# Kernel tuning notes

Hardware: AMD Instinct MI355X
Metric: run time of the kernel (lower is better)

The kernel has to match this reference:

```python
import jax, jax.numpy as jnp
import numpy as np

N, D, NH, NC, B, NL = 400, 256, 4, 2, 64, 2
HD = D // NH


def _ln(x, g, b, eps=1e-5):
    mu = x.mean(-1, keepdims=True)
    var = ((x - mu) ** 2).mean(-1, keepdims=True)
    return (x - mu) * jax.lax.rsqrt(var + eps) * g + b


def _mha(q, kv, wqkv, bqkv, wo, bo):
    # torch nn.MultiheadAttention (batch_first), eval mode
    wq, wk, wv = jnp.split(wqkv, 3, axis=0)
    bq, bk, bv = jnp.split(bqkv, 3, axis=0)
    Bsz, Sq, _ = q.shape
    Sk = kv.shape[1]
    qh = (q @ wq.T + bq).reshape(Bsz, Sq, NH, HD).transpose(0, 2, 1, 3)
    kh = (kv @ wk.T + bk).reshape(Bsz, Sk, NH, HD).transpose(0, 2, 1, 3)
    vh = (kv @ wv.T + bv).reshape(Bsz, Sk, NH, HD).transpose(0, 2, 1, 3)
    scores = jnp.einsum('bhqd,bhkd->bhqk', qh, kh) / jnp.sqrt(jnp.float32(HD))
    attn = jax.nn.softmax(scores, axis=-1)
    o = jnp.einsum('bhqk,bhkd->bhqd', attn, vh)
    o = o.transpose(0, 2, 1, 3).reshape(Bsz, Sq, D)
    return o @ wo.T + bo


def setup_inputs() -> dict:
    key = jax.random.key(0)
    ks = iter(jax.random.split(key, 64))
    w = lambda *s: (jax.random.normal(next(ks), s, dtype=jnp.float32) * 0.02)
    inp = {
        'fc_matrix': jax.random.uniform(next(ks), (B, N, N), dtype=jnp.float32),
        'sc_matrix': jax.random.uniform(next(ks), (B, N, N), dtype=jnp.float32),
        'proj_w': w(D, N), 'proj_b': jnp.zeros((D,), jnp.float32),
        'enc_qkv_w': w(NL, 3 * D, D), 'enc_qkv_b': jnp.zeros((NL, 3 * D), jnp.float32),
        'enc_out_w': w(NL, D, D), 'enc_out_b': jnp.zeros((NL, D), jnp.float32),
        'enc_lin1_w': w(NL, 4 * D, D), 'enc_lin1_b': jnp.zeros((NL, 4 * D), jnp.float32),
        'enc_lin2_w': w(NL, D, 4 * D), 'enc_lin2_b': jnp.zeros((NL, D), jnp.float32),
        'enc_n1_g': jnp.ones((NL, D), jnp.float32), 'enc_n1_b': jnp.zeros((NL, D), jnp.float32),
        'enc_n2_g': jnp.ones((NL, D), jnp.float32), 'enc_n2_b': jnp.zeros((NL, D), jnp.float32),
        'gcn_w1': w(D, N), 'gcn_b1': jnp.zeros((D,), jnp.float32),
        'gcn_w2': w(D, D), 'gcn_b2': jnp.zeros((D,), jnp.float32),
        'ca1_qkv_w': w(3 * D, D), 'ca1_qkv_b': jnp.zeros((3 * D,), jnp.float32),
        'ca1_out_w': w(D, D), 'ca1_out_b': jnp.zeros((D,), jnp.float32),
        'ca1_n_g': jnp.ones((D,), jnp.float32), 'ca1_n_b': jnp.zeros((D,), jnp.float32),
        'ca2_qkv_w': w(3 * D, D), 'ca2_qkv_b': jnp.zeros((3 * D,), jnp.float32),
        'ca2_out_w': w(D, D), 'ca2_out_b': jnp.zeros((D,), jnp.float32),
        'ca2_n_g': jnp.ones((D,), jnp.float32), 'ca2_n_b': jnp.zeros((D,), jnp.float32),
        'cls_w1': w(128, N * D), 'cls_b1': jnp.zeros((128,), jnp.float32),
        'cls_w2': w(NC, 128), 'cls_b2': jnp.zeros((NC,), jnp.float32),
    }
    return inp


def reference(fc_matrix, sc_matrix, proj_w, proj_b,
              enc_qkv_w, enc_qkv_b, enc_out_w, enc_out_b,
              enc_lin1_w, enc_lin1_b, enc_lin2_w, enc_lin2_b,
              enc_n1_g, enc_n1_b, enc_n2_g, enc_n2_b,
              gcn_w1, gcn_b1, gcn_w2, gcn_b2,
              ca1_qkv_w, ca1_qkv_b, ca1_out_w, ca1_out_b, ca1_n_g, ca1_n_b,
              ca2_qkv_w, ca2_qkv_b, ca2_out_w, ca2_out_b, ca2_n_g, ca2_n_b,
              cls_w1, cls_b1, cls_w2, cls_b2):
    # ---- FC branch: input proj + 2 post-norm transformer encoder layers ----
    h = fc_matrix @ proj_w.T + proj_b  # [B,N,D]
    for l in range(NL):
        a = _mha(h, h, enc_qkv_w[l], enc_qkv_b[l], enc_out_w[l], enc_out_b[l])
        h = _ln(h + a, enc_n1_g[l], enc_n1_b[l])
        ff = jax.nn.relu(h @ enc_lin1_w[l].T + enc_lin1_b[l]) @ enc_lin2_w[l].T + enc_lin2_b[l]
        h = _ln(h + ff, enc_n2_g[l], enc_n2_b[l])
    Z_F = h

    # ---- SC branch: dense-equivalent of per-sample nonzero()+GCNConv ----
    # all entries of sc are nonzero -> edge set == dense adjacency (self-loops present,
    # so add_remaining_self_loops is a no-op). deg = in-degree (column sums of weights).
    deg = sc_matrix.sum(axis=-2)  # [B,N]
    dinv = jnp.where(deg > 0, jax.lax.rsqrt(deg), 0.0)
    An = dinv[:, :, None] * sc_matrix * dinv[:, None, :]  # An[b,i,j] = dinv_i * w_ij * dinv_j
    h1 = jnp.einsum('bij,bid->bjd', An, sc_matrix @ gcn_w1.T) + gcn_b1  # aggregate src->dst
    h1 = jax.nn.relu(h1)
    Z_S = jnp.einsum('bij,bid->bjd', An, h1 @ gcn_w2.T) + gcn_b2  # [B,N,D]

    # ---- Cross attention (eval: dropout = identity) ----
    Z_F_cross = _ln(Z_F + _mha(Z_F, Z_S, ca1_qkv_w, ca1_qkv_b, ca1_out_w, ca1_out_b), ca1_n_g, ca1_n_b)
    Z_S_cross = _ln(Z_S + _mha(Z_S, Z_F, ca2_qkv_w, ca2_qkv_b, ca2_out_w, ca2_out_b), ca2_n_g, ca2_n_b)

    Z_joint = (Z_F_cross + Z_S_cross) * 0.5
    flat = Z_joint.reshape(Z_joint.shape[0], -1)  # [B, N*D]
    logits = jax.nn.relu(flat @ cls_w1.T + cls_b1) @ cls_w2.T + cls_b2
    return logits
```

## Files before the change

kernel.cpp:

```cpp
#include <hip/hip_runtime.h>
#include <math.h>

#define NB   64
#define NN   400
#define DD   256
#define NHH  4
#define HDD  64
#define MR   25600

typedef __attribute__((ext_vector_type(8))) short bf16x8;
typedef __attribute__((ext_vector_type(4))) float f32x4;

__device__ __forceinline__ short f2bf(float x) {
    union { float f; unsigned u; } v; v.f = x;
    return (short)((v.u + 0x7FFFu + ((v.u >> 16) & 1u)) >> 16);
}
__device__ __forceinline__ float bf2f(short s) {
    union { unsigned u; float f; } v; v.u = ((unsigned)(unsigned short)s) << 16;
    return v.f;
}
__device__ __forceinline__ void gl_lds16(const void* g, void* l) {
    __builtin_amdgcn_global_load_lds(
        (const __attribute__((address_space(1))) unsigned*)g,
        (__attribute__((address_space(3))) unsigned*)l, 16, 0, 0);
}


__global__ __launch_bounds__(256) void gemm_p8(
    const short* __restrict__ A, int arows, long long sA,
    const short* __restrict__ B, int brows, long long sB,
    const float* __restrict__ bias,
    short* __restrict__ C, int crows, int crz, long long sCe,
    int M, int N, int Npad, int K, int relu)
{
    __shared__ short lds[17408];
    const int tid = threadIdx.x;
    const int z = blockIdx.z;
    const int m0 = blockIdx.x * 128, n0 = blockIdx.y * 128;
    const short* Ab = A + (size_t)z * sA;
    const short* Bb = B + (size_t)z * sB;

    const int w = tid >> 6, lane = tid & 63;
    const int quad = lane >> 4, l15 = lane & 15;
    const int wm = w & 1, wn = w >> 1;

    f32x4 acc[4][4] = {};

    const int KT = K >> 5;

    auto STAGE = [&](int buf, int kt) {
        const int gp0 = kt << 2;
        short* Al = lds + buf * 8192;
        short* Bl = Al + 4096;
#pragma unroll
        for (int i = 0; i < 4; ++i) {
            int c = i * 4 + w;
            int p = (c >> 1) & 3, hh = c & 1;
            if (c < 8)
                gl_lds16(Ab + ((size_t)(gp0 + p) * arows + m0 + hh * 64 + lane) * 8,
                         &Al[(p * 128 + hh * 64) * 8]);
            else
                gl_lds16(Bb + ((size_t)(gp0 + p) * brows + n0 + hh * 64 + lane) * 8,
                         &Bl[(p * 128 + hh * 64) * 8]);
        }
    };

    STAGE(0, 0);
    __syncthreads();
    for (int kt = 0; kt < KT; ++kt) {
        if (kt + 1 < KT) STAGE((kt + 1) & 1, kt + 1);
        const short* Al = lds + (kt & 1) * 8192;
        const short* Bl = Al + 4096;
        bf16x8 af[4], bfr[4];
#pragma unroll
        for (int mi = 0; mi < 4; ++mi)
            af[mi] = *reinterpret_cast<const bf16x8*>(
                &Al[(quad * 128 + wm * 64 + mi * 16 + l15) * 8]);
#pragma unroll
        for (int ni = 0; ni < 4; ++ni)
            bfr[ni] = *reinterpret_cast<const bf16x8*>(
                &Bl[(quad * 128 + wn * 64 + ni * 16 + l15) * 8]);
#pragma unroll
        for (int mi = 0; mi < 4; ++mi)
#pragma unroll
            for (int ni = 0; ni < 4; ++ni)
                acc[mi][ni] = __builtin_amdgcn_mfma_f32_16x16x32_bf16(af[mi], bfr[ni], acc[mi][ni], 0, 0, 0);
        __syncthreads();
    }

#pragma unroll
    for (int mi = 0; mi < 4; ++mi) {
#pragma unroll
        for (int r = 0; r < 4; ++r) {
            int row = wm * 64 + mi * 16 + quad * 4 + r;
#pragma unroll
            for (int ni = 0; ni < 4; ++ni) {
                int col = wn * 64 + ni * 16 + l15;
                int gcol = n0 + col;
                float v = 0.0f;
                if (gcol < N) {
                    v = acc[mi][ni][r];
                    if (bias) v += bias[gcol];
                    if (relu) v = fmaxf(v, 0.0f);
                }
                lds[row * 136 + col] = f2bf(v);
            }
        }
    }
    __syncthreads();
    short* Cbz = C + (size_t)z * sCe;
    const long long zr = (long long)z * crz;
#pragma unroll
    for (int t = 0; t < 8; ++t) {
        int c = t * 256 + tid;
        int row = c & 127, p16 = c >> 7;
        int grow = m0 + row;
        int gcol0 = n0 + p16 * 8;
        if (grow < M && gcol0 < Npad) {
            bf16x8 v = *reinterpret_cast<const bf16x8*>(&lds[row * 136 + p16 * 8]);
            *reinterpret_cast<bf16x8*>(
                &Cbz[((size_t)(gcol0 >> 3) * crows + zr + grow) * 8]) = v;
        }
    }
}

__global__ __launch_bounds__(256) void gemm_ln(
    const short* __restrict__ A,
    const short* __restrict__ B, int brows,
    const float* __restrict__ bias,
    const short* __restrict__ resid,
    const float* __restrict__ g, const float* __restrict__ bb,
    short* __restrict__ out, int K)
{
    __shared__ short lds[20480];
    __shared__ float gs[256], bs[256], bi_s[256];
    __shared__ float red[2][4][64];
    const int tid = threadIdx.x;
    const int m0 = blockIdx.x * 64;
    const int w = tid >> 6, lane = tid & 63;
    const int quad = lane >> 4, l15 = lane & 15;
    gs[tid] = g[tid]; bs[tid] = bb[tid]; bi_s[tid] = bias[tid];

    f32x4 acc[16] = {};
    const int KT = K >> 5;

    auto STAGE = [&](int buf, int kt) {
        const int gp0 = kt << 2;
        short* Al = lds + buf * 10240;
        short* Bl = Al + 2048;
#pragma unroll
        for (int i = 0; i < 5; ++i) {
            int c = i * 4 + w;
            if (c < 4) {
                gl_lds16(A + ((size_t)(gp0 + c) * MR + m0 + lane) * 8, &Al[(c * 64) * 8]);
            } else {
                int cb = c - 4, p = cb >> 2, cq = cb & 3;
                gl_lds16(B + ((size_t)(gp0 + p) * brows + cq * 64 + lane) * 8,
                         &Bl[(p * 256 + cq * 64) * 8]);
            }
        }
    };

    STAGE(0, 0);
    __syncthreads();
    for (int kt = 0; kt < KT; ++kt) {
        if (kt + 1 < KT) STAGE((kt + 1) & 1, kt + 1);
        const short* Al = lds + (kt & 1) * 10240;
        const short* Bl = Al + 2048;
        bf16x8 af = *reinterpret_cast<const bf16x8*>(
            &Al[(quad * 64 + w * 16 + l15) * 8]);
#pragma unroll
        for (int ni = 0; ni < 16; ++ni) {
            bf16x8 bfr = *reinterpret_cast<const bf16x8*>(
                &Bl[(quad * 256 + ni * 16 + l15) * 8]);
            acc[ni] = __builtin_amdgcn_mfma_f32_16x16x32_bf16(af, bfr, acc[ni], 0, 0, 0);
        }
        __syncthreads();
    }

    short* rowt = lds;
#pragma unroll
    for (int ni = 0; ni < 16; ++ni) {
        int col = ni * 16 + l15;
        int part = col >> 6, idx = col & 63;
#pragma unroll
        for (int r = 0; r < 4; ++r) {
            int row = w * 16 + quad * 4 + r;
            rowt[row * 264 + part * 66 + idx] = f2bf(acc[ni][r] + bi_s[col]);
        }
    }
    __syncthreads();

    const int row = tid >> 2, part = tid & 3;
    const int grow = m0 + row;
    float vv[8][8];
    float sum = 0.0f, sq = 0.0f;
#pragma unroll
    for (int i = 0; i < 8; ++i) {
        int plane = part * 8 + i;
        bf16x8 rv = *reinterpret_cast<const bf16x8*>(resid + ((size_t)plane * MR + grow) * 8);
        bf16x8 tv = *reinterpret_cast<const bf16x8*>(&rowt[row * 264 + part * 66 + i * 8]);
#pragma unroll
        for (int e = 0; e < 8; ++e) {
            float v = bf2f(tv[e]) + bf2f(rv[e]);
            vv[i][e] = v; sum += v; sq += v * v;
        }
    }
    red[0][part][row] = sum; red[1][part][row] = sq;
    __syncthreads();
    sum = red[0][0][row] + red[0][1][row] + red[0][2][row] + red[0][3][row];
    sq  = red[1][0][row] + red[1][1][row] + red[1][2][row] + red[1][3][row];
    float mu = sum * (1.0f / 256.0f);
    float var = sq * (1.0f / 256.0f) - mu * mu;
    float rstd = 1.0f / sqrtf(fmaxf(var, 0.0f) + 1e-5f);
#pragma unroll
    for (int i = 0; i < 8; ++i) {
        int plane = part * 8 + i;
        bf16x8 o;
#pragma unroll
        for (int e = 0; e < 8; ++e)
            o[e] = f2bf((vv[i][e] - mu) * rstd * gs[plane * 8 + e] + bs[plane * 8 + e]);
        *reinterpret_cast<bf16x8*>(out + ((size_t)plane * MR + grow) * 8) = o;
    }
}

__global__ __launch_bounds__(256) void vtrans(
    const short* __restrict__ qkv, short* __restrict__ vT)
{
    __shared__ short tile[64][66];
    const int c = blockIdx.x, h = blockIdx.y, b = blockIdx.z;
    const int tid = threadIdx.x;
    const size_t bh = (size_t)b * NHH + h;
    for (int t = tid; t < 512; t += 256) {
        int pp = t >> 6, l = t & 63;
        int j = c * 64 + l;
        bf16x8 v;
        if (j < NN)
            v = *reinterpret_cast<const bf16x8*>(
                qkv + (((size_t)(64 + 8 * h + pp)) * MR + (size_t)b * NN + j) * 8);
        else { for (int e = 0; e < 8; ++e) v[e] = 0; }
#pragma unroll
        for (int e = 0; e < 8; ++e) tile[l][pp * 8 + e] = v[e];
    }
    __syncthreads();
    for (int t = tid; t < 512; t += 256) {
        int kq = t >> 6, d = t & 63;
        int kp = c * 8 + kq;
        bf16x8 o;
#pragma unroll
        for (int e = 0; e < 8; ++e) o[e] = tile[kq * 8 + e][d];
        *reinterpret_cast<bf16x8*>(vT + ((bh * 56 + kp) * 64 + d) * 8) = o;
    }
}

__global__ __launch_bounds__(256) void attn_p8(
    const short* __restrict__ qkv, const short* __restrict__ vT,
    short* __restrict__ Out)
{
    __shared__ short KP[8 * 448 * 8];
    __shared__ short QV[2][4096];
    const int qt = blockIdx.x, h = blockIdx.y, b = blockIdx.z;
    const int tid = threadIdx.x;
    const int w = tid >> 6, lane = tid & 63;
    const int quad = lane >> 4, l15 = lane & 15;
    const size_t rowb = (size_t)b * NN;
    const size_t bh = (size_t)b * NHH + h;

    for (int j = w; j < 8; j += 4)
        gl_lds16(qkv + (((size_t)(8 * h + j)) * MR + rowb + qt * 64 + lane) * 8, &QV[0][(j * 64) * 8]);
    for (int t = w; t < 56; t += 4) {
        int j = t / 7, c = t - j * 7;
        gl_lds16(qkv + (((size_t)(32 + 8 * h + j)) * MR + rowb + c * 64 + lane) * 8,
                 &KP[(j * 448 + c * 64) * 8]);
    }
    __syncthreads();

    bf16x8 aq0 = *reinterpret_cast<const bf16x8*>(&QV[0][(quad * 64 + w * 16 + l15) * 8]);
    bf16x8 aq1 = *reinterpret_cast<const bf16x8*>(&QV[0][((4 + quad) * 64 + w * 16 + l15) * 8]);
    __syncthreads();
    gl_lds16(vT + ((bh * 56 + w) * 64 + lane) * 8,       &QV[0][(w * 64) * 8]);
    gl_lds16(vT + ((bh * 56 + 4 + w) * 64 + lane) * 8,   &QV[0][((4 + w) * 64) * 8]);

    f32x4 sacc[25];
#pragma unroll
    for (int nt = 0; nt < 25; ++nt) { sacc[nt][0] = 0; sacc[nt][1] = 0; sacc[nt][2] = 0; sacc[nt][3] = 0; }
#pragma unroll
    for (int nt = 0; nt < 25; ++nt) {
        bf16x8 b0 = *reinterpret_cast<const bf16x8*>(&KP[(quad * 448 + nt * 16 + l15) * 8]);
        bf16x8 b1 = *reinterpret_cast<const bf16x8*>(&KP[((4 + quad) * 448 + nt * 16 + l15) * 8]);
        sacc[nt] = __builtin_amdgcn_mfma_f32_16x16x32_bf16(aq0, b0, sacc[nt], 0, 0, 0);
        sacc[nt] = __builtin_amdgcn_mfma_f32_16x16x32_bf16(aq1, b1, sacc[nt], 0, 0, 0);
    }

    float mx[4] = {-3e38f, -3e38f, -3e38f, -3e38f}, sm[4] = {0, 0, 0, 0};
#pragma unroll
    for (int nt = 0; nt < 25; ++nt)
#pragma unroll
        for (int r = 0; r < 4; ++r) mx[r] = fmaxf(mx[r], sacc[nt][r]);
#pragma unroll
    for (int r = 0; r < 4; ++r) {
        mx[r] = fmaxf(mx[r], __shfl_xor(mx[r], 1));
        mx[r] = fmaxf(mx[r], __shfl_xor(mx[r], 2));
        mx[r] = fmaxf(mx[r], __shfl_xor(mx[r], 4));
        mx[r] = fmaxf(mx[r], __shfl_xor(mx[r], 8));
    }
#pragma unroll
    for (int nt = 0; nt < 25; ++nt)
#pragma unroll
        for (int r = 0; r < 4; ++r) {
            float e = __expf((sacc[nt][r] - mx[r]) * 0.125f);
            sacc[nt][r] = e;
            sm[r] += e;
        }
#pragma unroll
    for (int r = 0; r < 4; ++r) {
        sm[r] += __shfl_xor(sm[r], 1);
        sm[r] += __shfl_xor(sm[r], 2);
        sm[r] += __shfl_xor(sm[r], 4);
        sm[r] += __shfl_xor(sm[r], 8);
    }
    __syncthreads();

#pragma unroll
    for (int nt = 0; nt < 25; ++nt)
#pragma unroll
        for (int r = 0; r < 4; ++r) {
            int colk = nt * 16 + l15;
            KP[((colk >> 3) * 64 + w * 16 + quad * 4 + r) * 8 + (colk & 7)] = f2bf(sacc[nt][r]);
        }
    for (int idx = tid; idx < 1024; idx += 256) KP[25600 + idx] = 0;

    f32x4 oacc[4];
#pragma unroll
    for (int dt = 0; dt < 4; ++dt) { oacc[dt][0] = 0; oacc[dt][1] = 0; oacc[dt][2] = 0; oacc[dt][3] = 0; }
    __syncthreads();

    for (int c2 = 0; c2 < 7; ++c2) {
        if (c2 < 6) {
            const int cp = (c2 + 1) * 8;
            short* dstv = QV[(c2 + 1) & 1];
            gl_lds16(vT + ((bh * 56 + cp + w) * 64 + lane) * 8,     &dstv[(w * 64) * 8]);
            gl_lds16(vT + ((bh * 56 + cp + 4 + w) * 64 + lane) * 8, &dstv[((4 + w) * 64) * 8]);
        }
        const short* Vb = QV[c2 & 1];
#pragma unroll
        for (int half = 0; half < 2; ++half) {
            const int kt = c2 * 2 + half;
            if (kt <= 12) {
                bf16x8 pa = *reinterpret_cast<const bf16x8*>(
                    &KP[((kt * 4 + quad) * 64 + w * 16 + l15) * 8]);
#pragma unroll
                for (int dt = 0; dt < 4; ++dt) {
                    bf16x8 vb = *reinterpret_cast<const bf16x8*>(
                        &Vb[((half * 4 + quad) * 64 + dt * 16 + l15) * 8]);
                    oacc[dt] = __builtin_amdgcn_mfma_f32_16x16x32_bf16(pa, vb, oacc[dt], 0, 0, 0);
                }
            }
        }
        if (c2 < 6) __syncthreads();
    }
#pragma unroll
    for (int r = 0; r < 4; ++r) {
        int row = qt * 64 + w * 16 + quad * 4 + r;
        if (row >= NN) continue;
        float inv = 1.0f / sm[r];
#pragma unroll
        for (int dt = 0; dt < 4; ++dt) {
            int col = dt * 16 + l15;
            Out[(((size_t)(8 * h + (col >> 3))) * MR + rowb + row) * 8 + (col & 7)] =
                f2bf(oacc[dt][r] * inv);
        }
    }
}

__global__ void conv_p8(const float* __restrict__ src, short* __restrict__ dst,
                        int R, int K, int Kp, int PR)
{
    const int G = Kp >> 3;
    int idx = blockIdx.x * 256 + threadIdx.x;
    if (idx >= R * G) return;
    int r = idx / G, g = idx - r * G;
    int k0 = g << 3;
    bf16x8 o;
    if (k0 + 8 <= K) {
        const float4 v0 = *reinterpret_cast<const float4*>(src + (size_t)r * K + k0);
        const float4 v1 = *reinterpret_cast<const float4*>(src + (size_t)r * K + k0 + 4);
        o[0] = f2bf(v0.x); o[1] = f2bf(v0.y); o[2] = f2bf(v0.z); o[3] = f2bf(v0.w);
        o[4] = f2bf(v1.x); o[5] = f2bf(v1.y); o[6] = f2bf(v1.z); o[7] = f2bf(v1.w);
    } else {
#pragma unroll
        for (int e = 0; e < 8; ++e) {
            int k = k0 + e;
            o[e] = (k < K) ? f2bf(src[(size_t)r * K + k]) : (short)0;
        }
    }
    *reinterpret_cast<bf16x8*>(dst + ((size_t)g * PR + r) * 8) = o;
}

__global__ __launch_bounds__(256) void w1_p8(
    const float* __restrict__ W1, short* __restrict__ Wp)
{
    __shared__ float tile[128][129];
    const int k0 = blockIdx.x * 128;
    const int tid = threadIdx.x;
    for (int t = 0; t < 16; ++t) {
        int idx = t * 256 + tid;
        int r = idx >> 5, k4 = idx & 31;
        float4 v = *(const float4*)(W1 + (size_t)r * 102400 + k0 + k4 * 4);
        tile[r][k4 * 4 + 0] = v.x; tile[r][k4 * 4 + 1] = v.y;
        tile[r][k4 * 4 + 2] = v.z; tile[r][k4 * 4 + 3] = v.w;
    }
    __syncthreads();
    for (int t = 0; t < 8; ++t) {
        int idx = t * 256 + tid;
        int pidx = idx >> 7, r = idx & 127;
        bf16x8 o;
#pragma unroll
        for (int e = 0; e < 8; ++e) o[e] = f2bf(tile[r][pidx * 8 + e]);
        *reinterpret_cast<bf16x8*>(Wp + (((size_t)(k0 >> 3) + pidx) * 128 + r) * 8) = o;
    }
}

__global__ void colsum_dinv(const float* __restrict__ sc, float* __restrict__ dinv)
{
    int b = blockIdx.y;
    int j = blockIdx.x * 256 + threadIdx.x;
    if (j >= NN) return;
    const float* p = sc + (size_t)b * NN * NN + j;
    float s = 0.0f;
    for (int i = 0; i < NN; ++i) s += p[(size_t)i * NN];
    dinv[b * NN + j] = (s > 0.0f) ? 1.0f / sqrtf(s) : 0.0f;
}

__global__ __launch_bounds__(256) void sc_prep(
    const float* __restrict__ sc, const float* __restrict__ dinv,
    short* __restrict__ scb, short* __restrict__ anT)
{
    __shared__ float tile[64][65];
    const int b = blockIdx.z;
    const int i0 = blockIdx.y * 64, j0 = blockIdx.x * 64;
    const int tid = threadIdx.x;
    const float* sb = sc + (size_t)b * NN * NN;
    short* scbb = scb + (size_t)b * 56 * 512 * 8;
    short* anTb = anT + (size_t)b * 56 * 512 * 8;
    for (int e = tid; e < 4096; e += 256) {
        int r = e >> 6, c = e & 63;
        int i = i0 + r, j = j0 + c;
        tile[r][c] = (i < NN && j < NN) ? sb[(size_t)i * NN + j] : 0.0f;
    }
    __syncthreads();
    for (int e = tid; e < 4096; e += 256) {
        int r = e >> 6, c = e & 63;
        int i = i0 + r, j = j0 + c;
        scbb[((size_t)(j >> 3) * 512 + i) * 8 + (j & 7)] = f2bf(tile[r][c]);
        float v = 0.0f;
        if (i < NN && j < NN) v = tile[r][c] * dinv[b * NN + i] * dinv[b * NN + j];
        anTb[((size_t)(i >> 3) * 512 + j) * 8 + (i & 7)] = f2bf(v);
    }
}

__global__ __launch_bounds__(256) void cls_gemm(
    const short* __restrict__ C1, const short* __restrict__ C2,
    const short* __restrict__ Wp, float* __restrict__ partial)
{
    __shared__ short Al[32 * 64 * 8];
    __shared__ short Wl[8 * 128 * 8];
    const int j = blockIdx.x;
    const int tid = threadIdx.x;
    const int w = tid >> 6, lane = tid & 63;
    const int quad = lane >> 4, l15 = lane & 15;

    for (int s = 0; s < 8; ++s) {
        int idx = s * 256 + tid;
        int p = idx >> 6, b = idx & 63;
        size_t ad = ((size_t)p * MR + (size_t)b * NN + j) * 8;
        bf16x8 a = *reinterpret_cast<const bf16x8*>(C1 + ad);
        bf16x8 c = *reinterpret_cast<const bf16x8*>(C2 + ad);
        bf16x8 o;
#pragma unroll
        for (int e = 0; e < 8; ++e) o[e] = f2bf(0.5f * (bf2f(a[e]) + bf2f(c[e])));
        *reinterpret_cast<bf16x8*>(&Al[(p * 64 + b) * 8]) = o;
    }

    f32x4 acc[4][2] = {};
    const size_t wp0 = (size_t)j * 32;
    for (int s = 0; s < 4; ++s) {
#pragma unroll
        for (int pp = 0; pp < 2; ++pp) {
            int p = w + pp * 4;
            gl_lds16(Wp + ((wp0 + s * 8 + p) * 128 + lane) * 8,      &Wl[(p * 128) * 8]);
            gl_lds16(Wp + ((wp0 + s * 8 + p) * 128 + 64 + lane) * 8, &Wl[(p * 128 + 64) * 8]);
        }
        __syncthreads();
#pragma unroll
        for (int kb = 0; kb < 2; ++kb) {
            bf16x8 af[4], bfr[2];
#pragma unroll
            for (int mi = 0; mi < 4; ++mi)
                af[mi] = *reinterpret_cast<const bf16x8*>(
                    &Al[((s * 8 + kb * 4 + quad) * 64 + mi * 16 + l15) * 8]);
#pragma unroll
            for (int ni = 0; ni < 2; ++ni)
                bfr[ni] = *reinterpret_cast<const bf16x8*>(
                    &Wl[((kb * 4 + quad) * 128 + w * 32 + ni * 16 + l15) * 8]);
#pragma unroll
            for (int mi = 0; mi < 4; ++mi)
#pragma unroll
                for (int ni = 0; ni < 2; ++ni)
                    acc[mi][ni] = __builtin_amdgcn_mfma_f32_16x16x32_bf16(af[mi], bfr[ni], acc[mi][ni], 0, 0, 0);
        }
        __syncthreads();
    }
    float* pj = partial + (size_t)j * 8192;
#pragma unroll
    for (int mi = 0; mi < 4; ++mi)
#pragma unroll
        for (int r = 0; r < 4; ++r) {
            int row = mi * 16 + quad * 4 + r;
#pragma unroll
            for (int ni = 0; ni < 2; ++ni)
                pj[row * 128 + w * 32 + ni * 16 + l15] = acc[mi][ni][r];
        }
}

__global__ void cls_reduce(const float* __restrict__ partial, float* __restrict__ clsh)
{
    int o = blockIdx.x * 256 + threadIdx.x;
    float s = 0.0f;
    for (int kb = 0; kb < 400; ++kb) s += partial[(size_t)kb * 8192 + o];
    clsh[o] = s;
}

__global__ void logits_final(
    const float* __restrict__ clsh, const float* __restrict__ b1,
    const float* __restrict__ w2, const float* __restrict__ b2,
    float* __restrict__ out)
{
    __shared__ float t[128];
    int b = blockIdx.x;
    int tid = threadIdx.x;
    t[tid] = fmaxf(clsh[b * 128 + tid] + b1[tid], 0.0f);
    __syncthreads();
    if (tid < 2) {
        float s = b2[tid];
        for (int o = 0; o < 128; ++o) s += t[o] * w2[tid * 128 + o];
        out[b * 2 + tid] = s;
    }
}

extern "C" void kernel_launch(void* const* d_in, const int* in_sizes, int n_in,
                              void* d_out, int out_size, void* d_ws, size_t ws_size,
                              hipStream_t stream)
{
    const float* fc        = (const float*)d_in[0];
    const float* sc        = (const float*)d_in[1];
    const float* proj_w    = (const float*)d_in[2];
    const float* proj_b    = (const float*)d_in[3];
    const float* enc_qkv_w = (const float*)d_in[4];
    const float* enc_qkv_b = (const float*)d_in[5];
    const float* enc_out_w = (const float*)d_in[6];
    const float* enc_out_b = (const float*)d_in[7];
    const float* enc_l1_w  = (const float*)d_in[8];
    const float* enc_l1_b  = (const float*)d_in[9];
    const float* enc_l2_w  = (const float*)d_in[10];
    const float* enc_l2_b  = (const float*)d_in[11];
    const float* enc_n1_g  = (const float*)d_in[12];
    const float* enc_n1_b  = (const float*)d_in[13];
    const float* enc_n2_g  = (const float*)d_in[14];
    const float* enc_n2_b  = (const float*)d_in[15];
    const float* gcn_w1    = (const float*)d_in[16];
    const float* gcn_b1    = (const float*)d_in[17];
    const float* gcn_w2    = (const float*)d_in[18];
    const float* gcn_b2    = (const float*)d_in[19];
    const float* ca1_qkv_w = (const float*)d_in[20];
    const float* ca1_qkv_b = (const float*)d_in[21];
    const float* ca1_out_w = (const float*)d_in[22];
    const float* ca1_out_b = (const float*)d_in[23];
    const float* ca1_n_g   = (const float*)d_in[24];
    const float* ca1_n_b   = (const float*)d_in[25];
    const float* ca2_qkv_w = (const float*)d_in[26];
    const float* ca2_qkv_b = (const float*)d_in[27];
    const float* ca2_out_w = (const float*)d_in[28];
    const float* ca2_out_b = (const float*)d_in[29];
    const float* ca2_n_g   = (const float*)d_in[30];
    const float* ca2_n_b   = (const float*)d_in[31];
    const float* cls_w1    = (const float*)d_in[32];
    const float* cls_b1    = (const float*)d_in[33];
    const float* cls_w2    = (const float*)d_in[34];
    const float* cls_b2    = (const float*)d_in[35];

    char* wsb = (char*)d_ws;
    size_t off = 0;
    auto alloc = [&](size_t bytes) { char* r = wsb + off; off += (bytes + 255) & ~(size_t)255; return r; };
    short* bufBig = (short*)alloc((size_t)MR * 1024 * 2);
    short* fcb    = (short*)alloc((size_t)56 * MR * 8 * 2);
    short* anT    = (short*)alloc((size_t)NB * 56 * 512 * 8 * 2);
    short* bufH   = (short*)alloc((size_t)32 * MR * 8 * 2);
    short* bufA   = (short*)alloc((size_t)32 * MR * 8 * 2);
    short* bufC   = (short*)alloc((size_t)32 * MR * 8 * 2);
    short* bufZS  = (short*)alloc((size_t)32 * MR * 8 * 2);
    short* vT     = (short*)alloc((size_t)NB * NHH * 56 * 64 * 8 * 2);
    short* w1b    = (short*)alloc((size_t)12800 * 128 * 8 * 2);
    short* projwb = (short*)alloc((size_t)56 * 256 * 8 * 2);
    short* qkvwb  = (short*)alloc((size_t)32 * 1536 * 8 * 2);
    short* outwb  = (short*)alloc((size_t)32 * 512 * 8 * 2);
    short* l1wb   = (short*)alloc((size_t)32 * 2048 * 8 * 2);
    short* l2wb   = (short*)alloc((size_t)128 * 512 * 8 * 2);
    short* gw1b   = (short*)alloc((size_t)56 * 256 * 8 * 2);
    short* gw2b   = (short*)alloc((size_t)32 * 256 * 8 * 2);
    short* c1qb   = (short*)alloc((size_t)32 * 768 * 8 * 2);
    short* c1ob   = (short*)alloc((size_t)32 * 256 * 8 * 2);
    short* c2qb   = (short*)alloc((size_t)32 * 768 * 8 * 2);
    short* c2ob   = (short*)alloc((size_t)32 * 256 * 8 * 2);
    float* dinv   = (float*)alloc((size_t)MR * 4);
    float* clsh   = (float*)alloc((size_t)NB * 128 * 4);
    short* scb = bufBig;
    short* XT1 = bufBig + (size_t)64 * 56 * 512 * 8;
    short* h1  = bufBig;
    short* XT2 = XT1;
    float* partial = (float*)fcb;

    dim3 blk(256);
    auto cgrid = [](long long n) { return dim3((unsigned)((n + 255) / 256)); };

    conv_p8<<<cgrid((long long)MR * 56), blk, 0, stream>>>(fc, fcb, MR, 400, 448, MR);
    conv_p8<<<cgrid(256 * 56), blk, 0, stream>>>(proj_w, projwb, 256, 400, 448, 256);
    conv_p8<<<cgrid(1536 * 32), blk, 0, stream>>>(enc_qkv_w, qkvwb, 1536, 256, 256, 1536);
    conv_p8<<<cgrid(512 * 32), blk, 0, stream>>>(enc_out_w, outwb, 512, 256, 256, 512);
    conv_p8<<<cgrid(2048 * 32), blk, 0, stream>>>(enc_l1_w, l1wb, 2048, 256, 256, 2048);
    conv_p8<<<cgrid(512 * 128), blk, 0, stream>>>(enc_l2_w, l2wb, 512, 1024, 1024, 512);
    conv_p8<<<cgrid(256 * 56), blk, 0, stream>>>(gcn_w1, gw1b, 256, 400, 448, 256);
    conv_p8<<<cgrid(256 * 32), blk, 0, stream>>>(gcn_w2, gw2b, 256, 256, 256, 256);
    conv_p8<<<cgrid(768 * 32), blk, 0, stream>>>(ca1_qkv_w, c1qb, 768, 256, 256, 768);
    conv_p8<<<cgrid(256 * 32), blk, 0, stream>>>(ca1_out_w, c1ob, 256, 256, 256, 256);
    conv_p8<<<cgrid(768 * 32), blk, 0, stream>>>(ca2_qkv_w, c2qb, 768, 256, 256, 768);
    conv_p8<<<cgrid(256 * 32), blk, 0, stream>>>(ca2_out_w, c2ob, 256, 256, 256, 256);
    w1_p8<<<800, blk, 0, stream>>>(cls_w1, w1b);

    gemm_p8<<<dim3(200, 2, 1), blk, 0, stream>>>(
        fcb, MR, 0, projwb, 256, 0, proj_b, bufH, MR, 0, 0, MR, 256, 256, 448, 0);
    for (int l = 0; l < 2; ++l) {
        gemm_p8<<<dim3(200, 6, 1), blk, 0, stream>>>(
            bufH, MR, 0, qkvwb + (size_t)l * 768 * 8, 1536, 0, enc_qkv_b + l * 768,
            bufBig, MR, 0, 0, MR, 768, 768, 256, 0);
        vtrans<<<dim3(7, NHH, NB), blk, 0, stream>>>(bufBig, vT);
        attn_p8<<<dim3(7, NHH, NB), blk, 0, stream>>>(bufBig, vT, bufA);
        gemm_ln<<<400, blk, 0, stream>>>(
            bufA, outwb + (size_t)l * 256 * 8, 512, enc_out_b + l * 256,
            bufH, enc_n1_g + l * DD, enc_n1_b + l * DD, bufH, 256);
        gemm_p8<<<dim3(200, 8, 1), blk, 0, stream>>>(
            bufH, MR, 0, l1wb + (size_t)l * 1024 * 8, 2048, 0, enc_l1_b + l * 1024,
            bufBig, MR, 0, 0, MR, 1024, 1024, 256, 1);
        gemm_ln<<<400, blk, 0, stream>>>(
            bufBig, l2wb + (size_t)l * 256 * 8, 512, enc_l2_b + l * 256,
            bufH, enc_n2_g + l * DD, enc_n2_b + l * DD, bufH, 1024);
    }

    colsum_dinv<<<dim3(2, NB), blk, 0, stream>>>(sc, dinv);
    sc_prep<<<dim3(7, 7, NB), blk, 0, stream>>>(sc, dinv, scb, anT);
    gemm_p8<<<dim3(2, 4, NB), blk, 0, stream>>>(
        gw1b, 256, 0, scb, 512, 56LL * 512 * 8, nullptr,
        XT1, 256, 0, 56LL * 256 * 8, 256, 400, 448, 448, 0);
    gemm_p8<<<dim3(4, 2, NB), blk, 0, stream>>>(
        anT, 512, 56LL * 512 * 8, XT1, 256, 56LL * 256 * 8, gcn_b1,
        h1, 512, 0, 32LL * 512 * 8, 400, 256, 256, 448, 1);
    gemm_p8<<<dim3(2, 4, NB), blk, 0, stream>>>(
        gw2b, 256, 0, h1, 512, 32LL * 512 * 8, nullptr,
        XT2, 256, 0, 56LL * 256 * 8, 256, 400, 448, 256, 0);
    gemm_p8<<<dim3(4, 2, NB), blk, 0, stream>>>(
        anT, 512, 56LL * 512 * 8, XT2, 256, 56LL * 256 * 8, gcn_b2,
        bufZS, MR, 400, 0, 400, 256, 256, 448, 0);

    gemm_p8<<<dim3(200, 2, 1), blk, 0, stream>>>(
        bufH, MR, 0, c1qb, 768, 0, ca1_qkv_b, bufBig, MR, 0, 0, MR, 256, 256, 256, 0);
    gemm_p8<<<dim3(200, 4, 1), blk, 0, stream>>>(
        bufZS, MR, 0, c1qb + 256 * 8, 768, 0, ca1_qkv_b + 256,
        bufBig + (size_t)32 * MR * 8, MR, 0, 0, MR, 512, 512, 256, 0);
    vtrans<<<dim3(7, NHH, NB), blk, 0, stream>>>(bufBig, vT);
    attn_p8<<<dim3(7, NHH, NB), blk, 0, stream>>>(bufBig, vT, bufA);
    gemm_ln<<<400, blk, 0, stream>>>(
        bufA, c1ob, 256, ca1_out_b, bufH, ca1_n_g, ca1_n_b, bufC, 256);

    gemm_p8<<<dim3(200, 2, 1), blk, 0, stream>>>(
        bufZS, MR, 0, c2qb, 768, 0, ca2_qkv_b, bufBig, MR, 0, 0, MR, 256, 256, 256, 0);
    gemm_p8<<<dim3(200, 4, 1), blk, 0, stream>>>(
        bufH, MR, 0, c2qb + 256 * 8, 768, 0, ca2_qkv_b + 256,
        bufBig + (size_t)32 * MR * 8, MR, 0, 0, MR, 512, 512, 256, 0);
    vtrans<<<dim3(7, NHH, NB), blk, 0, stream>>>(bufBig, vT);
    attn_p8<<<dim3(7, NHH, NB), blk, 0, stream>>>(bufBig, vT, bufA);
    gemm_ln<<<400, blk, 0, stream>>>(
        bufA, c2ob, 256, ca2_out_b, bufZS, ca2_n_g, ca2_n_b, bufZS, 256);

    cls_gemm<<<400, blk, 0, stream>>>(bufC, bufZS, w1b, partial);
    cls_reduce<<<32, blk, 0, stream>>>(partial, clsh);
    logits_final<<<NB, 128, 0, stream>>>(clsh, cls_b1, cls_w2, cls_b2, (float*)d_out);
}
```

Baseline: 1.058 ms.

## Triple-buffer GEMM loads with vmcnt waits and XCD-aware attention block mapping

The GEMM and GEMM+LayerNorm kernels move from double to triple buffering. Two stages are prefetched, and the loop waits only on vmcnt counts, with one raw barrier per iteration in place of two __syncthreads. The attention kernel now streams V in 13 finer chunks through a 5-slot ring with counted waits. vtrans and attention use a flat grid remapped so that the 7 tiles of a batch-head share one XCD, for L2 locality. These changes raise LDS use per block, which may lower occupancy, and they rely on correct hand-tuned vmcnt counts.

```diff
diff --git a/kernel.cpp b/kernel.cpp
--- a/kernel.cpp
+++ b/kernel.cpp
@@ -24,6 +24,21 @@
         (const __attribute__((address_space(1))) unsigned*)g,
         (__attribute__((address_space(3))) unsigned*)l, 16, 0, 0);
 }
+__device__ __forceinline__ void wait_vmcnt(int n) {
+    switch (n) {
+    case 0: asm volatile("s_waitcnt vmcnt(0)" ::: "memory"); break;
+    case 1: asm volatile("s_waitcnt vmcnt(1)" ::: "memory"); break;
+    case 2: asm volatile("s_waitcnt vmcnt(2)" ::: "memory"); break;
+    case 3: asm volatile("s_waitcnt vmcnt(3)" ::: "memory"); break;
+    case 4: asm volatile("s_waitcnt vmcnt(4)" ::: "memory"); break;
+    default: asm volatile("s_waitcnt vmcnt(5)" ::: "memory"); break;
+    }
+}
+__device__ __forceinline__ void barrier_raw() {
+    __builtin_amdgcn_sched_barrier(0);
+    __builtin_amdgcn_s_barrier();
+    __builtin_amdgcn_sched_barrier(0);
+}
 
 
 __global__ __launch_bounds__(256) void gemm_p8(
@@ -33,7 +48,7 @@
     short* __restrict__ C, int crows, int crz, long long sCe,
     int M, int N, int Npad, int K, int relu)
 {
-    __shared__ short lds[17408];
+    __shared__ short lds[24576];
     const int tid = threadIdx.x;
     const int z = blockIdx.z;
     const int m0 = blockIdx.x * 128, n0 = blockIdx.y * 128;
@@ -66,10 +81,12 @@
     };
 
     STAGE(0, 0);
-    __syncthreads();
+    STAGE(1, 1);
     for (int kt = 0; kt < KT; ++kt) {
-        if (kt + 1 < KT) STAGE((kt + 1) & 1, kt + 1);
-        const short* Al = lds + (kt & 1) * 8192;
+        wait_vmcnt(kt + 1 < KT ? 4 : 0);
+        barrier_raw();
+        if (kt + 2 < KT) STAGE((kt + 2) % 3, kt + 2);
+        const short* Al = lds + (kt % 3) * 8192;
         const short* Bl = Al + 4096;
         bf16x8 af[4], bfr[4];
 #pragma unroll
@@ -85,8 +102,8 @@
 #pragma unroll
             for (int ni = 0; ni < 4; ++ni)
                 acc[mi][ni] = __builtin_amdgcn_mfma_f32_16x16x32_bf16(af[mi], bfr[ni], acc[mi][ni], 0, 0, 0);
-        __syncthreads();
-    }
+    }
+    __syncthreads();
 
 #pragma unroll
     for (int mi = 0; mi < 4; ++mi) {
@@ -132,7 +149,7 @@
     const float* __restrict__ g, const float* __restrict__ bb,
     short* __restrict__ out, int K)
 {
-    __shared__ short lds[20480];
+    __shared__ short lds[30720];
     __shared__ float gs[256], bs[256], bi_s[256];
     __shared__ float red[2][4][64];
     const int tid = threadIdx.x;
@@ -162,10 +179,12 @@
     };
 
     STAGE(0, 0);
-    __syncthreads();
+    STAGE(1, 1);
     for (int kt = 0; kt < KT; ++kt) {
-        if (kt + 1 < KT) STAGE((kt + 1) & 1, kt + 1);
-        const short* Al = lds + (kt & 1) * 10240;
+        wait_vmcnt(kt + 1 < KT ? 5 : 0);
+        barrier_raw();
+        if (kt + 2 < KT) STAGE((kt + 2) % 3, kt + 2);
+        const short* Al = lds + (kt % 3) * 10240;
         const short* Bl = Al + 2048;
         bf16x8 af = *reinterpret_cast<const bf16x8*>(
             &Al[(quad * 64 + w * 16 + l15) * 8]);
@@ -175,8 +194,8 @@
                 &Bl[(quad * 256 + ni * 16 + l15) * 8]);
             acc[ni] = __builtin_amdgcn_mfma_f32_16x16x32_bf16(af, bfr, acc[ni], 0, 0, 0);
         }
-        __syncthreads();
-    }
+    }
+    __syncthreads();
 
     short* rowt = lds;
 #pragma unroll
@@ -228,9 +247,13 @@
     const short* __restrict__ qkv, short* __restrict__ vT)
 {
     __shared__ short tile[64][66];
-    const int c = blockIdx.x, h = blockIdx.y, b = blockIdx.z;
+    const int id = blockIdx.x;
+    const int xcd = id & 7, rem = id >> 3;
+    const int bh_hi = rem / 7, c = rem - bh_hi * 7;
+    const int bh_i = bh_hi * 8 + xcd;
+    const int h = bh_i & 3, b = bh_i >> 2;
     const int tid = threadIdx.x;
-    const size_t bh = (size_t)b * NHH + h;
+    const size_t bh = (size_t)bh_i;
     for (int t = tid; t < 512; t += 256) {
         int pp = t >> 6, l = t & 63;
         int j = c * 64 + l;
@@ -258,16 +281,20 @@
     short* __restrict__ Out)
 {
     __shared__ short KP[8 * 448 * 8];
-    __shared__ short QV[2][4096];
-    const int qt = blockIdx.x, h = blockIdx.y, b = blockIdx.z;
+    __shared__ short QV[5][2048];
+    const int id = blockIdx.x;
+    const int xcd = id & 7, rem = id >> 3;
+    const int bh_hi = rem / 7, qt = rem - bh_hi * 7;
+    const int bh_i = bh_hi * 8 + xcd;
+    const int h = bh_i & 3, b = bh_i >> 2;
     const int tid = threadIdx.x;
     const int w = tid >> 6, lane = tid & 63;
     const int quad = lane >> 4, l15 = lane & 15;
     const size_t rowb = (size_t)b * NN;
-    const size_t bh = (size_t)b * NHH + h;
-
+
+    short* Qs = &QV[0][0];
     for (int j = w; j < 8; j += 4)
-        gl_lds16(qkv + (((size_t)(8 * h + j)) * MR + rowb + qt * 64 + lane) * 8, &QV[0][(j * 64) * 8]);
+        gl_lds16(qkv + (((size_t)(8 * h + j)) * MR + rowb + qt * 64 + lane) * 8, &Qs[j * 512]);
     for (int t = w; t < 56; t += 4) {
         int j = t / 7, c = t - j * 7;
         gl_lds16(qkv + (((size_t)(32 + 8 * h + j)) * MR + rowb + c * 64 + lane) * 8,
@@ -275,11 +302,12 @@
     }
     __syncthreads();
 
-    bf16x8 aq0 = *reinterpret_cast<const bf16x8*>(&QV[0][(quad * 64 + w * 16 + l15) * 8]);
-    bf16x8 aq1 = *reinterpret_cast<const bf16x8*>(&QV[0][((4 + quad) * 64 + w * 16 + l15) * 8]);
-    __syncthreads();
-    gl_lds16(vT + ((bh * 56 + w) * 64 + lane) * 8,       &QV[0][(w * 64) * 8]);
-    gl_lds16(vT + ((bh * 56 + 4 + w) * 64 + lane) * 8,   &QV[0][((4 + w) * 64) * 8]);
+    bf16x8 aq0 = *reinterpret_cast<const bf16x8*>(&Qs[(quad * 64 + w * 16 + l15) * 8]);
+    bf16x8 aq1 = *reinterpret_cast<const bf16x8*>(&Qs[((4 + quad) * 64 + w * 16 + l15) * 8]);
+    __syncthreads();
+#pragma unroll
+    for (int c = 0; c < 4; ++c)
+        gl_lds16(vT + (((size_t)bh_i * 56 + c * 4 + w) * 64 + lane) * 8, &QV[c][w * 512]);
 
     f32x4 sacc[25];
 #pragma unroll
@@ -335,29 +363,21 @@
     for (int dt = 0; dt < 4; ++dt) { oacc[dt][0] = 0; oacc[dt][1] = 0; oacc[dt][2] = 0; oacc[dt][3] = 0; }
     __syncthreads();
 
-    for (int c2 = 0; c2 < 7; ++c2) {
-        if (c2 < 6) {
-            const int cp = (c2 + 1) * 8;
-            short* dstv = QV[(c2 + 1) & 1];
-            gl_lds16(vT + ((bh * 56 + cp + w) * 64 + lane) * 8,     &dstv[(w * 64) * 8]);
-            gl_lds16(vT + ((bh * 56 + cp + 4 + w) * 64 + lane) * 8, &dstv[((4 + w) * 64) * 8]);
-        }
-        const short* Vb = QV[c2 & 1];
-#pragma unroll
-        for (int half = 0; half < 2; ++half) {
-            const int kt = c2 * 2 + half;
-            if (kt <= 12) {
-                bf16x8 pa = *reinterpret_cast<const bf16x8*>(
-                    &KP[((kt * 4 + quad) * 64 + w * 16 + l15) * 8]);
-#pragma unroll
-                for (int dt = 0; dt < 4; ++dt) {
-                    bf16x8 vb = *reinterpret_cast<const bf16x8*>(
-                        &Vb[((half * 4 + quad) * 64 + dt * 16 + l15) * 8]);
-                    oacc[dt] = __builtin_amdgcn_mfma_f32_16x16x32_bf16(pa, vb, oacc[dt], 0, 0, 0);
-                }
-            }
-        }
-        if (c2 < 6) __syncthreads();
+#pragma unroll
+    for (int c = 0; c < 13; ++c) {
+        wait_vmcnt((12 - c) < 3 ? (12 - c) : 3);
+        barrier_raw();
+        if (c + 4 <= 12)
+            gl_lds16(vT + (((size_t)bh_i * 56 + (c + 4) * 4 + w) * 64 + lane) * 8,
+                     &QV[(c + 4) % 5][w * 512]);
+        bf16x8 pa = *reinterpret_cast<const bf16x8*>(
+            &KP[((c * 4 + quad) * 64 + w * 16 + l15) * 8]);
+#pragma unroll
+        for (int dt = 0; dt < 4; ++dt) {
+            bf16x8 vb = *reinterpret_cast<const bf16x8*>(
+                &QV[c % 5][quad * 512 + (dt * 16 + l15) * 8]);
+            oacc[dt] = __builtin_amdgcn_mfma_f32_16x16x32_bf16(pa, vb, oacc[dt], 0, 0, 0);
+        }
     }
 #pragma unroll
     for (int r = 0; r < 4; ++r) {
@@ -643,8 +663,8 @@
         gemm_p8<<<dim3(200, 6, 1), blk, 0, stream>>>(
             bufH, MR, 0, qkvwb + (size_t)l * 768 * 8, 1536, 0, enc_qkv_b + l * 768,
             bufBig, MR, 0, 0, MR, 768, 768, 256, 0);
-        vtrans<<<dim3(7, NHH, NB), blk, 0, stream>>>(bufBig, vT);
-        attn_p8<<<dim3(7, NHH, NB), blk, 0, stream>>>(bufBig, vT, bufA);
+        vtrans<<<dim3(1792), blk, 0, stream>>>(bufBig, vT);
+        attn_p8<<<dim3(1792), blk, 0, stream>>>(bufBig, vT, bufA);
         gemm_ln<<<400, blk, 0, stream>>>(
             bufA, outwb + (size_t)l * 256 * 8, 512, enc_out_b + l * 256,
             bufH, enc_n1_g + l * DD, enc_n1_b + l * DD, bufH, 256);
@@ -676,8 +696,8 @@
     gemm_p8<<<dim3(200, 4, 1), blk, 0, stream>>>(
         bufZS, MR, 0, c1qb + 256 * 8, 768, 0, ca1_qkv_b + 256,
         bufBig + (size_t)32 * MR * 8, MR, 0, 0, MR, 512, 512, 256, 0);
-    vtrans<<<dim3(7, NHH, NB), blk, 0, stream>>>(bufBig, vT);
-    attn_p8<<<dim3(7, NHH, NB), blk, 0, stream>>>(bufBig, vT, bufA);
+    vtrans<<<dim3(1792), blk, 0, stream>>>(bufBig, vT);
+    attn_p8<<<dim3(1792), blk, 0, stream>>>(bufBig, vT, bufA);
     gemm_ln<<<400, blk, 0, stream>>>(
         bufA, c1ob, 256, ca1_out_b, bufH, ca1_n_g, ca1_n_b, bufC, 256);
 
@@ -686,8 +706,8 @@
     gemm_p8<<<dim3(200, 4, 1), blk, 0, stream>>>(
         bufH, MR, 0, c2qb + 256 * 8, 768, 0, ca2_qkv_b + 256,
         bufBig + (size_t)32 * MR * 8, MR, 0, 0, MR, 512, 512, 256, 0);
-    vtrans<<<dim3(7, NHH, NB), blk, 0, stream>>>(bufBig, vT);
-    attn_p8<<<dim3(7, NHH, NB), blk, 0, stream>>>(bufBig, vT, bufA);
+    vtrans<<<dim3(1792), blk, 0, stream>>>(bufBig, vT);
+    attn_p8<<<dim3(1792), blk, 0, stream>>>(bufBig, vT, bufA);
     gemm_ln<<<400, blk, 0, stream>>>(
         bufA, c2ob, 256, ca2_out_b, bufZS, ca2_n_g, ca2_n_b, bufZS, 256);
 
```

After: 1.020 ms. 1.04x faster.
